# Kernel optimization log

Hardware: AMD Instinct MI355X
Metric: run time of the kernel (lower is better)

## Reference

```python
import jax, jax.numpy as jnp
import numpy as np

B, T, D = 32, 256, 1024      # batch, seq_len, input_size
H = D // 2                   # LSTM hidden size = 512
K = 128                      # num_tags


def setup_inputs() -> dict:
    key = jax.random.key(0)
    ks = jax.random.split(key, 16)
    s_in = 1.0 / np.sqrt(D + K)
    s_h = 1.0 / np.sqrt(H)
    return {
        "hiddens": jax.random.normal(ks[0], (B, T, D), jnp.float32),
        "h_t": jax.random.normal(ks[1], (2, B, H), jnp.float32),
        "c_t": jax.random.normal(ks[2], (2, B, H), jnp.float32),
        "mask": jnp.ones((B, T), jnp.float32),
        # output layer: Linear(H, K)
        "W_out": jax.random.normal(ks[3], (K, H), jnp.float32) * s_h,
        "b_out": jnp.zeros((K,), jnp.float32),
        # LSTM layer 0: input dim = K + D
        "W_ih0": jax.random.normal(ks[4], (4 * H, K + D), jnp.float32) * s_in,
        "W_hh0": jax.random.normal(ks[5], (4 * H, H), jnp.float32) * s_h,
        "b_ih0": jnp.zeros((4 * H,), jnp.float32),
        "b_hh0": jnp.zeros((4 * H,), jnp.float32),
        # LSTM layer 1: input dim = H
        "W_ih1": jax.random.normal(ks[6], (4 * H, H), jnp.float32) * s_h,
        "W_hh1": jax.random.normal(ks[7], (4 * H, H), jnp.float32) * s_h,
        "b_ih1": jnp.zeros((4 * H,), jnp.float32),
        "b_hh1": jnp.zeros((4 * H,), jnp.float32),
    }


def _lstm_cell(x, h, c, W_ih, W_hh, b_ih, b_hh):
    g = x @ W_ih.T + h @ W_hh.T + b_ih + b_hh
    i, f, gg, o = jnp.split(g, 4, axis=-1)
    i = jax.nn.sigmoid(i); f = jax.nn.sigmoid(f)
    gg = jnp.tanh(gg); o = jax.nn.sigmoid(o)
    c = f * c + i * gg
    h = o * jnp.tanh(c)
    return h, c


def reference(hiddens, h_t, c_t, mask, W_out, b_out,
              W_ih0, W_hh0, b_ih0, b_hh0, W_ih1, W_hh1, b_ih1, b_hh1):
    # initial previous-tag distribution from first frame's first half
    last_tag = hiddens[:, 0, :H] @ W_out.T + b_out          # [B,K]
    sm = jax.nn.softmax(last_tag, axis=-1)

    def step(carry, x_t):
        h1, c1, h2, c2, sm = carry
        inp = jnp.concatenate([x_t, sm], axis=-1)           # [B, D+K]
        h1, c1 = _lstm_cell(inp, h1, c1, W_ih0, W_hh0, b_ih0, b_hh0)
        h2, c2 = _lstm_cell(h1, h2, c2, W_ih1, W_hh1, b_ih1, b_hh1)
        logit = h2 @ W_out.T + b_out                        # [B,K]
        sm = jax.nn.softmax(logit, axis=-1)
        return (h1, c1, h2, c2, sm), logit

    carry0 = (h_t[0], c_t[0], h_t[1], c_t[1], sm)
    _, logits_t = jax.lax.scan(step, carry0, jnp.swapaxes(hiddens, 0, 1))  # [T,B,K]
    logits = jnp.swapaxes(logits_t, 0, 1)                   # [B,T,K]
    logits = logits + (1.0 - mask)[:, :, None] * jnp.float32(-1e32)
    prob = jax.nn.softmax(logits, axis=-1)
    return prob
```

## Files before the change

kernel.cpp:

```cpp
#include <hip/hip_runtime.h>
#include <cstdint>
#include <cstddef>


#define Bz   32
#define Tz   256
#define Dz   1024
#define Hz   512
#define NK   128
#define IN0  1152
#define NBLK 256
#define BH   16384

typedef float vf4 __attribute__((ext_vector_type(4)));

__device__ __forceinline__ void ldsc4(vf4& d, const float* p) {
  asm volatile("global_load_dwordx4 %0, %1, off sc0 sc1" : "=v"(d) : "v"(p));
}
__device__ __forceinline__ void ldg1(float& d, const float* p) {
  asm volatile("global_load_dword %0, %1, off" : "=v"(d) : "v"(p));
}
__device__ __forceinline__ void stsc1(float* p, float v) {
  asm volatile("global_store_dword %0, %1, off sc0 sc1" :: "v"(p), "v"(v) : "memory");
}
__device__ __forceinline__ void stsc1u(unsigned int* p, unsigned int v) {
  asm volatile("global_store_dword %0, %1, off sc0 sc1" :: "v"(p), "v"(v) : "memory");
}
#define FENCE8(c, a0,a1,a2,a3,a4,a5,a6,a7) \
  asm volatile("s_waitcnt vmcnt(" #c ")" : "+v"(a0),"+v"(a1),"+v"(a2),"+v"(a3), \
               "+v"(a4),"+v"(a5),"+v"(a6),"+v"(a7) :: "memory")

#define FMA4(acc, W_, A_) \
  acc = fmaf((W_).x,(A_).x, fmaf((W_).y,(A_).y, fmaf((W_).z,(A_).z, fmaf((W_).w,(A_).w,(acc)))))

__device__ __forceinline__ float sigf(float x) { return 1.0f / (1.0f + expf(-x)); }

__device__ __forceinline__ void gbar(unsigned int* slots, unsigned int* bcast,
                                     int gidx, bool master, unsigned int g) {
  asm volatile("s_waitcnt vmcnt(0)" ::: "memory");
  __syncthreads();
  if (threadIdx.x == 0)
    __hip_atomic_store(slots + gidx * 16, g,
                       __ATOMIC_RELAXED, __HIP_MEMORY_SCOPE_SYSTEM);
  if (master) {
    if (threadIdx.x < 128) {
      unsigned int* wsl = slots + threadIdx.x * 16;
      while (__hip_atomic_load(wsl, __ATOMIC_RELAXED, __HIP_MEMORY_SCOPE_SYSTEM) < g)
        __builtin_amdgcn_s_sleep(1);
    }
    __syncthreads();
    if (threadIdx.x == 0) {
      asm volatile("s_waitcnt vmcnt(0)" ::: "memory");
      __hip_atomic_store(bcast, g, __ATOMIC_RELAXED, __HIP_MEMORY_SCOPE_SYSTEM);
    }
  } else if (threadIdx.x == 0) {
    while (__hip_atomic_load(bcast, __ATOMIC_RELAXED, __HIP_MEMORY_SCOPE_SYSTEM) < g)
      __builtin_amdgcn_s_sleep(1);
  }
  __syncthreads();
}

__device__ __forceinline__ void garrive(unsigned int* slots, int gidx,
                                        unsigned int g) {
  asm volatile("s_waitcnt vmcnt(0)" ::: "memory");
  __syncthreads();
  if (threadIdx.x == 0)
    __hip_atomic_store(slots + gidx * 16, g,
                       __ATOMIC_RELAXED, __HIP_MEMORY_SCOPE_SYSTEM);
}

#define FMAROW(r, AV, BASE, KOFF) \
  { vf4 wv = *(const vf4*)&BASE[r][KOFF]; FMA4(A##r, wv, AV); }
#define R16A(OP, AV, BASE, KOFF) \
  OP(0,AV,BASE,KOFF) OP(1,AV,BASE,KOFF) OP(2,AV,BASE,KOFF) OP(3,AV,BASE,KOFF) \
  OP(4,AV,BASE,KOFF) OP(5,AV,BASE,KOFF) OP(6,AV,BASE,KOFF) OP(7,AV,BASE,KOFF) \
  OP(8,AV,BASE,KOFF) OP(9,AV,BASE,KOFF) OP(10,AV,BASE,KOFF) OP(11,AV,BASE,KOFF) \
  OP(12,AV,BASE,KOFF) OP(13,AV,BASE,KOFF) OP(14,AV,BASE,KOFF) OP(15,AV,BASE,KOFF)

#define RED16 { \
  { const bool hi = (ks & 1) != 0; \
    float s0=hi?A0:A8, s1=hi?A1:A9, s2=hi?A2:A10, s3=hi?A3:A11; \
    float s4=hi?A4:A12, s5=hi?A5:A13, s6=hi?A6:A14, s7=hi?A7:A15; \
    float k0=hi?A8:A0, k1=hi?A9:A1, k2=hi?A10:A2, k3=hi?A11:A3; \
    float k4=hi?A12:A4, k5=hi?A13:A5, k6=hi?A14:A6, k7=hi?A15:A7; \
    A0=k0+__shfl_xor(s0,1,64); A1=k1+__shfl_xor(s1,1,64); \
    A2=k2+__shfl_xor(s2,1,64); A3=k3+__shfl_xor(s3,1,64); \
    A4=k4+__shfl_xor(s4,1,64); A5=k5+__shfl_xor(s5,1,64); \
    A6=k6+__shfl_xor(s6,1,64); A7=k7+__shfl_xor(s7,1,64); } \
  { const bool hi = (ks & 2) != 0; \
    float s0=hi?A0:A4, s1=hi?A1:A5, s2=hi?A2:A6, s3=hi?A3:A7; \
    float k0=hi?A4:A0, k1=hi?A5:A1, k2=hi?A6:A2, k3=hi?A7:A3; \
    A0=k0+__shfl_xor(s0,2,64); A1=k1+__shfl_xor(s1,2,64); \
    A2=k2+__shfl_xor(s2,2,64); A3=k3+__shfl_xor(s3,2,64); } \
  { const bool hi = (ks & 4) != 0; \
    float s0=hi?A0:A2, s1=hi?A1:A3; float k0=hi?A2:A0, k1=hi?A3:A1; \
    A0=k0+__shfl_xor(s0,4,64); A1=k1+__shfl_xor(s1,4,64); } \
  { const bool hi = (ks & 8) != 0; \
    float s0=hi?A0:A1; float k0=hi?A1:A0; \
    A0=k0+__shfl_xor(s0,8,64); } }

#define ZERO16 A0=0.f;A1=0.f;A2=0.f;A3=0.f;A4=0.f;A5=0.f;A6=0.f;A7=0.f; \
               A8=0.f;A9=0.f;A10=0.f;A11=0.f;A12=0.f;A13=0.f;A14=0.f;A15=0.f;

#define GATES(CREG, HDST) \
  __syncthreads(); \
  if (tid < 64) { \
    float gi = gbuf[cu][cbl],      gf = gbuf[4 + cu][cbl]; \
    float gg = gbuf[8 + cu][cbl],  go = gbuf[12 + cu][cbl]; \
    CREG = sigf(gf) * CREG + sigf(gi) * tanhf(gg); \
    stsc1(HDST + (size_t)(pg * 16 + cbl) * Hz + jg * 4 + cu, \
          sigf(go) * tanhf(CREG)); \
  }

__device__ void c_head_crit(const float* src, int bb,
                            const float* __restrict__ W_out,
                            const float* __restrict__ b_out,
                            float* __restrict__ smg, float* __restrict__ lggb,
                            float (*cpart)[2], float* wred,
                            unsigned int* smflag, unsigned int fval) {
  const int tid = threadIdx.x;
  const int n = tid & 127, kh = tid >> 7;
  float p = 0.0f;
  const float* w  = W_out + (size_t)n * Hz + kh * 256;
  const float* s2 = src + kh * 256;
  #pragma unroll 8
  for (int k = 0; k < 256; k += 4) {
    vf4 sv = *(const vf4*)(s2 + k);
    vf4 wv = *(const vf4*)(w + k);
    p += sv.x * wv.x + sv.y * wv.y + sv.z * wv.z + sv.w * wv.w;
  }
  cpart[n][kh] = p;
  __syncthreads();
  float logit = 0.0f;
  if (tid < 128) {
    logit = cpart[n][0] + cpart[n][1] + b_out[n];
    stsc1(lggb + n, logit);
  }
  float e = (tid < 128) ? expf(logit) : 0.0f;
  float s = e;
  #pragma unroll
  for (int off = 32; off >= 1; off >>= 1) s += __shfl_xor(s, off);
  if ((tid & 63) == 0 && tid < 128) wred[2 + (tid >> 6)] = s;
  __syncthreads();
  float S = wred[2] + wred[3];
  if (tid < 128) stsc1(smg + bb * NK + n, e / S);
  asm volatile("s_waitcnt vmcnt(0)" ::: "memory");
  __syncthreads();
  if (fval && tid == 0) stsc1u(smflag, fval);
}

__device__ void c_head_out(int t, int bb, const float* __restrict__ mask,
                           float* __restrict__ out,
                           const float* __restrict__ lggb, float* wred) {
  const int tid = threadIdx.x;
  const int n = tid & 127;
  float lg = 0.0f;
  if (tid < 128)
    lg = __hip_atomic_load(lggb + n, __ATOMIC_RELAXED, __HIP_MEMORY_SCOPE_SYSTEM);
  float mk = (tid < 128) ? mask[bb * Tz + t] : 1.0f;
  float lm = (tid < 128) ? (lg + (1.0f - mk) * (-1e32f)) : -3.0e38f;
  float m2 = lm;
  #pragma unroll
  for (int off = 32; off >= 1; off >>= 1) m2 = fmaxf(m2, __shfl_xor(m2, off));
  if ((tid & 63) == 0 && tid < 128) wred[4 + (tid >> 6)] = m2;
  __syncthreads();
  float M2 = fmaxf(wred[4], wred[5]);
  float e2 = (tid < 128) ? expf(lm - M2) : 0.0f;
  float s2r = e2;
  #pragma unroll
  for (int off = 32; off >= 1; off >>= 1) s2r += __shfl_xor(s2r, off);
  if ((tid & 63) == 0 && tid < 128) wred[6 + (tid >> 6)] = s2r;
  __syncthreads();
  float S2 = wred[6] + wred[7];
  if (tid < 128) out[((size_t)bb * Tz + t) * NK + n] = e2 / S2;
}

__global__ void __launch_bounds__(256)
xpre_kernel(const float* __restrict__ hiddens, const float* __restrict__ W_ih0,
            const float* __restrict__ b_ih0, const float* __restrict__ b_hh0,
            float* __restrict__ Xpre, int t0, int colTiles, int cstride) {
  __shared__ float Ws[16][64];
  __shared__ float Hs[16][64];
  const int tid = threadIdx.x;
  const int bx = blockIdx.x % colTiles;
  const int by = blockIdx.x / colTiles;
  const int n0 = by * 64, c0 = bx * 64;
  const int tx = tid & 15, ty = tid >> 4;
  const int ldn = tid >> 2;
  const int ldk = (tid & 3) * 4;

  const int bb = ldn & 31;
  const int tt = t0 + (c0 >> 5) + (ldn >> 5);
  const float* hsrc = hiddens + ((size_t)bb * Tz + tt) * Dz + ldk;
  const float* wsrc = W_ih0 + (size_t)(n0 + ldn) * IN0 + ldk;

  float acc[4][4] = {};
  vf4 wv = *(const vf4*)(wsrc);
  vf4 hv = *(const vf4*)(hsrc);
  for (int k0 = 0; k0 < Dz; k0 += 16) {
    __syncthreads();
    Ws[ldk + 0][ldn] = wv.x; Ws[ldk + 1][ldn] = wv.y;
    Ws[ldk + 2][ldn] = wv.z; Ws[ldk + 3][ldn] = wv.w;
    Hs[ldk + 0][ldn] = hv.x; Hs[ldk + 1][ldn] = hv.y;
    Hs[ldk + 2][ldn] = hv.z; Hs[ldk + 3][ldn] = hv.w;
    __syncthreads();
    if (k0 + 16 < Dz) {
      wv = *(const vf4*)(wsrc + k0 + 16);
      hv = *(const vf4*)(hsrc + k0 + 16);
    }
    #pragma unroll
    for (int k = 0; k < 16; ++k) {
      vf4 a4 = *(const vf4*)&Ws[k][ty * 4];
      vf4 b4 = *(const vf4*)&Hs[k][tx * 4];
      acc[0][0] += a4.x * b4.x; acc[0][1] += a4.x * b4.y; acc[0][2] += a4.x * b4.z; acc[0][3] += a4.x * b4.w;
      acc[1][0] += a4.y * b4.x; acc[1][1] += a4.y * b4.y; acc[1][2] += a4.y * b4.z; acc[1][3] += a4.y * b4.w;
      acc[2][0] += a4.z * b4.x; acc[2][1] += a4.z * b4.y; acc[2][2] += a4.z * b4.z; acc[2][3] += a4.z * b4.w;
      acc[3][0] += a4.w * b4.x; acc[3][1] += a4.w * b4.y; acc[3][2] += a4.w * b4.z; acc[3][3] += a4.w * b4.w;
    }
  }
  #pragma unroll
  for (int i = 0; i < 4; ++i) {
    int n = n0 + ty * 4 + i;
    float bi = b_ih0[n] + b_hh0[n];
    vf4 v; v.x = acc[i][0] + bi; v.y = acc[i][1] + bi;
    v.z = acc[i][2] + bi; v.w = acc[i][3] + bi;
    *(vf4*)(Xpre + (size_t)n * cstride + c0 + tx * 4) = v;
  }
}

__global__ void __launch_bounds__(256)
seq_kernel(const float* __restrict__ hiddens,
           const float* __restrict__ h_t, const float* __restrict__ c_t,
           const float* __restrict__ mask,
           const float* __restrict__ W_out, const float* __restrict__ b_out,
           const float* __restrict__ W_ih0, const float* __restrict__ W_hh0,
           const float* __restrict__ W_ih1, const float* __restrict__ W_hh1,
           const float* __restrict__ b_ih1, const float* __restrict__ b_hh1,
           const float* __restrict__ Xpre, float* __restrict__ out,
           float* __restrict__ h1g, float* __restrict__ h2g,
           float* __restrict__ smg, float* __restrict__ c1g, float* __restrict__ c2g,
           float* __restrict__ lgg,
           unsigned int* bar, int t0, int nsteps, int cstride) {
  __shared__ float wA[16][640];
  __shared__ float wB[16][1024];
  __shared__ float gbuf[16][17];
  __shared__ float biasB[16];
  __shared__ float hsg[512];
  __shared__ float cpart[128][2];
  __shared__ float wred[8];

  const int tid = threadIdx.x;
  const int bid = blockIdx.x;
  const int jg  = bid >> 1;
  const int pg  = bid & 1;
  const int ks  = tid & 15;
  const int bbl = tid >> 4;
  const int bbg = pg * 16 + bbl;
  const int ks4 = ks * 4;
  const int cu  = tid & 3, cbl = tid >> 2;
  const int rr  = ((ks & 1) << 3) | ((ks & 2) << 1) | ((ks & 4) >> 1) | ((ks & 8) >> 3);
  const int rowG = ((rr >> 2) * Hz) + jg * 4 + (rr & 3);
  const int hb = ((bid & 1) << 4) | (bid >> 1);
  const bool isbud = (bid >= 32 && bid < 64);
  const int  bb2   = isbud ? (((bid & 1) << 4) | ((bid >> 1) - 16)) : 0;

  unsigned int* barg = bar + pg * 2048;
  unsigned int* bcst = bar + 4096 + pg * 16;
  unsigned int* smf  = bar + 4608;
  const int  gidx    = bid >> 1;
  const bool gmaster = (gidx == 127);

  #pragma clang loop unroll(disable)
  for (int r = 0; r < 16; ++r) {
    const int row = ((r >> 2) * Hz) + jg * 4 + (r & 3);
    if (tid * 4 < 512)
      *(vf4*)&wA[r][tid * 4] = *(const vf4*)(W_hh0 + (size_t)row * Hz + tid * 4);
    if (tid * 4 < 128)
      *(vf4*)&wA[r][512 + tid * 4] = *(const vf4*)(W_ih0 + (size_t)row * IN0 + 1024 + tid * 4);
    if (tid * 4 < 512) {
      *(vf4*)&wB[r][tid * 4]       = *(const vf4*)(W_ih1 + (size_t)row * Hz + tid * 4);
      *(vf4*)&wB[r][512 + tid * 4] = *(const vf4*)(W_hh1 + (size_t)row * Hz + tid * 4);
    }
  }
  if (tid < 16) {
    const int row = ((tid >> 2) * Hz) + jg * 4 + (tid & 3);
    biasB[tid] = b_ih1[row] + b_hh1[row];
  }

  float c1r = 0.0f, c2r = 0.0f;
  if (tid < 64) {
    const size_t ci = (size_t)(pg * 16 + cbl) * Hz + jg * 4 + cu;
    if (t0 == 0) { c1r = c_t[ci]; c2r = c_t[BH + ci]; }
    else         { c1r = c1g[ci]; c2r = c2g[ci]; }
  }

  if (t0 == 0) {
    if (bid < 32 && tid < 128) {
      vf4 v1 = *(const vf4*)(h_t + (size_t)hb * Hz + tid * 4);
      vf4 v2 = *(const vf4*)(h_t + BH + (size_t)hb * Hz + tid * 4);
      float* d1 = h1g + BH + (size_t)hb * Hz + tid * 4;
      float* d2 = h2g + BH + (size_t)hb * Hz + tid * 4;
      stsc1(d1, v1.x); stsc1(d1 + 1, v1.y); stsc1(d1 + 2, v1.z); stsc1(d1 + 3, v1.w);
      stsc1(d2, v2.x); stsc1(d2 + 1, v2.y); stsc1(d2 + 2, v2.z); stsc1(d2 + 3, v2.w);
    }
    if (bid < 32) {
      if (tid < 128)
        *(vf4*)&hsg[tid * 4] = *(const vf4*)(hiddens + (size_t)hb * Tz * Dz + tid * 4);
      __syncthreads();
      c_head_crit(hsg, hb, W_out, b_out, smg, lgg + hb * NK, cpart, wred,
                  smf + hb * 16, 0u);
    }
  }
  __syncthreads();
  unsigned int g = 1;
  gbar(barg, bcst, gidx, gmaster, g); ++g;

  vf4 ca0,ca1,ca2,ca3,ca4,ca5,ca6,ca7;
  {
    const float* hp = h1g + ((t0 + 1) & 1) * BH + (size_t)bbg * Hz + ks4;
    ldsc4(ca0, hp);        ldsc4(ca1, hp + 64);  ldsc4(ca2, hp + 128);
    ldsc4(ca3, hp + 192);  ldsc4(ca4, hp + 256); ldsc4(ca5, hp + 320);
    ldsc4(ca6, hp + 384);  ldsc4(ca7, hp + 448);
    FENCE8(0, ca0,ca1,ca2,ca3,ca4,ca5,ca6,ca7);
  }

  #pragma clang loop unroll(disable)
  for (int k = 0; k < nsteps; ++k) {
    const int t = t0 + k;
    float*       h1cur  = h1g + (t & 1) * BH;
    const float* h2prev = h2g + ((t + 1) & 1) * BH;
    float*       h2cur  = h2g + (t & 1) * BH;
    float A0,A1,A2,A3,A4,A5,A6,A7,A8,A9,A10,A11,A12,A13,A14,A15;
    vf4 ab0,ab1,ab2,ab3,ab4,ab5,ab6,ab7;

    {
      vf4 as0,as1;
      float xv;
      ldg1(xv, Xpre + (size_t)rowG * cstride + k * 32 + bbg);
      ZERO16
      R16A(FMAROW, ca0, wA, ks4 +   0)
      R16A(FMAROW, ca1, wA, ks4 +  64)
      R16A(FMAROW, ca2, wA, ks4 + 128)
      R16A(FMAROW, ca3, wA, ks4 + 192)
      R16A(FMAROW, ca4, wA, ks4 + 256)
      R16A(FMAROW, ca5, wA, ks4 + 320)
      R16A(FMAROW, ca6, wA, ks4 + 384)
      R16A(FMAROW, ca7, wA, ks4 + 448)
      RED16
      const float partA = A0;
      if (k > 0) {
        const unsigned int tgt = (unsigned int)k;
        if (tid < 16) {
          const unsigned int* fp = smf + (pg * 16 + tid) * 16;
          while (__hip_atomic_load(fp, __ATOMIC_RELAXED,
                                   __HIP_MEMORY_SCOPE_SYSTEM) < tgt)
            __builtin_amdgcn_s_sleep(1);
        }
        __syncthreads();
        if (isbud)
          c_head_out(t - 1, bb2, mask, out, lgg + bb2 * NK, wred);
      }
      const float* sp = smg + (size_t)bbg * NK + ks4;
      ldsc4(as0, sp);        ldsc4(as1, sp + 64);
      ZERO16
      asm volatile("s_waitcnt vmcnt(0)" : "+v"(as0), "+v"(as1), "+v"(xv) :: "memory");
      R16A(FMAROW, as0, wA, ks4 + 512)
      R16A(FMAROW, as1, wA, ks4 + 576)
      RED16
      gbuf[rr][bbl] = partA + A0 + xv;
      GATES(c1r, h1cur)
    }
    {
      const float* p2 = h2prev + (size_t)bbg * Hz + ks4;
      ldsc4(ab0, p2);       ldsc4(ab1, p2 + 64);  ldsc4(ab2, p2 + 128);
      ldsc4(ab3, p2 + 192); ldsc4(ab4, p2 + 256); ldsc4(ab5, p2 + 320);
      ldsc4(ab6, p2 + 384); ldsc4(ab7, p2 + 448);
    }
    const unsigned int gA = g;
    garrive(barg, gidx, gA); ++g;

    {
      ZERO16
      FENCE8(0, ab0,ab1,ab2,ab3,ab4,ab5,ab6,ab7);
      R16A(FMAROW, ab0, wB, ks4 + 512)
      R16A(FMAROW, ab1, wB, ks4 + 576)
      R16A(FMAROW, ab2, wB, ks4 + 640)
      R16A(FMAROW, ab3, wB, ks4 + 704)
      R16A(FMAROW, ab4, wB, ks4 + 768)
      R16A(FMAROW, ab5, wB, ks4 + 832)
      R16A(FMAROW, ab6, wB, ks4 + 896)
      R16A(FMAROW, ab7, wB, ks4 + 960)
      RED16
      const float partB = A0;
      if (gmaster) {
        if (tid < 128) {
          unsigned int* wsl = barg + tid * 16;
          while (__hip_atomic_load(wsl, __ATOMIC_RELAXED,
                                   __HIP_MEMORY_SCOPE_SYSTEM) < gA)
            __builtin_amdgcn_s_sleep(1);
        }
        __syncthreads();
        if (tid == 0)
          __hip_atomic_store(bcst, gA, __ATOMIC_RELAXED, __HIP_MEMORY_SCOPE_SYSTEM);
      } else if (tid == 0) {
        while (__hip_atomic_load(bcst, __ATOMIC_RELAXED,
                                 __HIP_MEMORY_SCOPE_SYSTEM) < gA)
          __builtin_amdgcn_s_sleep(1);
      }
      __syncthreads();
      const float* p1 = h1cur + (size_t)bbg * Hz + ks4;
      ldsc4(ca0, p1);       ldsc4(ca1, p1 + 64);  ldsc4(ca2, p1 + 128);
      ldsc4(ca3, p1 + 192); ldsc4(ca4, p1 + 256); ldsc4(ca5, p1 + 320);
      ldsc4(ca6, p1 + 384); ldsc4(ca7, p1 + 448);
      ZERO16
      FENCE8(0, ca0,ca1,ca2,ca3,ca4,ca5,ca6,ca7);
      R16A(FMAROW, ca0, wB, ks4 +   0)
      R16A(FMAROW, ca1, wB, ks4 +  64)
      R16A(FMAROW, ca2, wB, ks4 + 128)
      R16A(FMAROW, ca3, wB, ks4 + 192)
      R16A(FMAROW, ca4, wB, ks4 + 256)
      R16A(FMAROW, ca5, wB, ks4 + 320)
      R16A(FMAROW, ca6, wB, ks4 + 384)
      R16A(FMAROW, ca7, wB, ks4 + 448)
      RED16
      gbuf[rr][bbl] = A0 + partB + biasB[rr];
      GATES(c2r, h2cur)
    }
    const unsigned int gB = g;
    garrive(barg, gidx, gB); ++g;

    if (bid < 32) {
      if (tid < 128) {
        unsigned int* wsl = barg + tid * 16;
        while (__hip_atomic_load(wsl, __ATOMIC_RELAXED,
                                 __HIP_MEMORY_SCOPE_SYSTEM) < gB)
          __builtin_amdgcn_s_sleep(1);
      }
      __syncthreads();
      if (tid < 128) {
        vf4 v;
        ldsc4(v, h2cur + (size_t)hb * Hz + tid * 4);
        asm volatile("s_waitcnt vmcnt(0)" : "+v"(v) :: "memory");
        *(vf4*)&hsg[tid * 4] = v;
      }
      __syncthreads();
      c_head_crit(hsg, hb, W_out, b_out, smg, lgg + hb * NK, cpart, wred,
                  smf + hb * 16, (unsigned int)(k + 1));
    }
  }

  if (isbud) {
    if (tid == 0) {
      const unsigned int* fp = smf + bb2 * 16;
      while (__hip_atomic_load(fp, __ATOMIC_RELAXED,
                               __HIP_MEMORY_SCOPE_SYSTEM) < (unsigned int)nsteps)
        __builtin_amdgcn_s_sleep(1);
    }
    __syncthreads();
    c_head_out(t0 + nsteps - 1, bb2, mask, out, lgg + bb2 * NK, wred);
  }

  if (tid < 64) {
    const size_t ci = (size_t)(pg * 16 + cbl) * Hz + jg * 4 + cu;
    stsc1(c1g + ci, c1r);
    stsc1(c2g + ci, c2r);
  }
}

extern "C" void kernel_launch(void* const* d_in, const int* in_sizes, int n_in,
                              void* d_out, int out_size, void* d_ws, size_t ws_size,
                              hipStream_t stream) {
  (void)in_sizes; (void)n_in; (void)out_size;
  const float* hiddens = (const float*)d_in[0];
  const float* h_t     = (const float*)d_in[1];
  const float* c_t     = (const float*)d_in[2];
  const float* mask    = (const float*)d_in[3];
  const float* W_out   = (const float*)d_in[4];
  const float* b_out   = (const float*)d_in[5];
  const float* W_ih0   = (const float*)d_in[6];
  const float* W_hh0   = (const float*)d_in[7];
  const float* b_ih0   = (const float*)d_in[8];
  const float* b_hh0   = (const float*)d_in[9];
  const float* W_ih1   = (const float*)d_in[10];
  const float* W_hh1   = (const float*)d_in[11];
  const float* b_ih1   = (const float*)d_in[12];
  const float* b_hh1   = (const float*)d_in[13];
  float* out = (float*)d_out;

  unsigned int* bar = (unsigned int*)d_ws;
  float* base = (float*)((char*)d_ws + 32768);
  float* h1g  = base;
  float* h2g  = h1g + 2 * BH;
  float* smg  = h2g + 2 * BH;
  float* c1g  = smg + Bz * NK;
  float* c2g  = c1g + BH;
  float* lgg  = c2g + BH;
  float* Xpre = lgg + Bz * NK;

  const size_t fullNeed = 32768 + (size_t)(102400 + Bz * NK + 2048 * 8192) * 4;
  const bool full = ws_size >= fullNeed;
  const int NCH    = full ? 1 : 16;
  const int CH     = full ? Tz : 16;
  const int cstr   = full ? (Tz * 32) : (16 * 32);
  const int cTiles = cstr / 64;

  for (int c = 0; c < NCH; ++c) {
    const int t0 = c * CH;
    hipMemsetAsync(bar, 0, 32768, stream);
    hipLaunchKernelGGL(xpre_kernel, dim3(32 * cTiles), dim3(256), 0, stream,
                       hiddens, W_ih0, b_ih0, b_hh0, Xpre, t0, cTiles, cstr);
    int nsteps = CH, cs = cstr, tt0 = t0;
    void* ka[] = { (void*)&hiddens, (void*)&h_t, (void*)&c_t, (void*)&mask,
                   (void*)&W_out, (void*)&b_out, (void*)&W_ih0, (void*)&W_hh0,
                   (void*)&W_ih1, (void*)&W_hh1, (void*)&b_ih1, (void*)&b_hh1,
                   (void*)&Xpre, (void*)&out, (void*)&h1g, (void*)&h2g,
                   (void*)&smg, (void*)&c1g, (void*)&c2g, (void*)&lgg,
                   (void*)&bar, (void*)&tt0, (void*)&nsteps, (void*)&cs };
    hipError_t err = hipLaunchCooperativeKernel((void*)seq_kernel, dim3(NBLK),
                                                dim3(256), ka, 0, stream);
    if (err != hipSuccess) {
      hipLaunchKernelGGL(seq_kernel, dim3(NBLK), dim3(256), 0, stream,
                         hiddens, h_t, c_t, mask, W_out, b_out, W_ih0, W_hh0,
                         W_ih1, W_hh1, b_ih1, b_hh1, Xpre, out,
                         h1g, h2g, smg, c1g, c2g, lgg, bar, tt0, nsteps, cs);
    }
  }
}
```

Before: 5.256 ms.

## Defer softmax normalization into layer-0 gate input via packed flag+sum

The head block now writes unnormalized exp(logit) values and the softmax denominator. The denominator is packed into the 64-bit ready flag next to the step counter. Consumers read the sum along with the flag and scale their partial dot product by 1/S, which takes the division and a block barrier off the critical head path. The head's dot-product reduction also uses a lane shuffle instead of shared memory plus __syncthreads. The risk is that exp(logit) without max subtraction can overflow, and the 64-bit flag store must be atomic.

```diff
diff --git a/kernel.cpp b/kernel.cpp
--- a/kernel.cpp
+++ b/kernel.cpp
@@ -13,6 +13,7 @@
 #define BH   16384
 
 typedef float vf4 __attribute__((ext_vector_type(4)));
+typedef unsigned long long ull;
 
 __device__ __forceinline__ void ldsc4(vf4& d, const float* p) {
   asm volatile("global_load_dwordx4 %0, %1, off sc0 sc1" : "=v"(d) : "v"(p));
@@ -20,11 +21,17 @@
 __device__ __forceinline__ void ldg1(float& d, const float* p) {
   asm volatile("global_load_dword %0, %1, off" : "=v"(d) : "v"(p));
 }
+__device__ __forceinline__ float ldsc1f(const float* p) {
+  float d;
+  asm volatile("global_load_dword %0, %1, off sc0 sc1" : "=v"(d) : "v"(p));
+  asm volatile("s_waitcnt vmcnt(0)" : "+v"(d) :: "memory");
+  return d;
+}
 __device__ __forceinline__ void stsc1(float* p, float v) {
   asm volatile("global_store_dword %0, %1, off sc0 sc1" :: "v"(p), "v"(v) : "memory");
 }
-__device__ __forceinline__ void stsc1u(unsigned int* p, unsigned int v) {
-  asm volatile("global_store_dword %0, %1, off sc0 sc1" :: "v"(p), "v"(v) : "memory");
+__device__ __forceinline__ void stsc2u(ull* p, ull v) {
+  asm volatile("global_store_dwordx2 %0, %1, off sc0 sc1" :: "v"(p), "v"(v) : "memory");
 }
 #define FENCE8(c, a0,a1,a2,a3,a4,a5,a6,a7) \
   asm volatile("s_waitcnt vmcnt(" #c ")" : "+v"(a0),"+v"(a1),"+v"(a2),"+v"(a3), \
@@ -116,10 +123,10 @@
                             const float* __restrict__ W_out,
                             const float* __restrict__ b_out,
                             float* __restrict__ smg, float* __restrict__ lggb,
-                            float (*cpart)[2], float* wred,
-                            unsigned int* smflag, unsigned int fval) {
+                            float* __restrict__ sSb, float* wred,
+                            ull* smflag64, unsigned int fval) {
   const int tid = threadIdx.x;
-  const int n = tid & 127, kh = tid >> 7;
+  const int n = tid >> 1, kh = tid & 1;
   float p = 0.0f;
   const float* w  = W_out + (size_t)n * Hz + kh * 256;
   const float* s2 = src + kh * 256;
@@ -129,24 +136,26 @@
     vf4 wv = *(const vf4*)(w + k);
     p += sv.x * wv.x + sv.y * wv.y + sv.z * wv.z + sv.w * wv.w;
   }
-  cpart[n][kh] = p;
-  __syncthreads();
-  float logit = 0.0f;
-  if (tid < 128) {
-    logit = cpart[n][0] + cpart[n][1] + b_out[n];
+  p += __shfl_xor(p, 1, 64);
+  float logit = p + b_out[n];
+  float e = expf(logit);
+  if (kh == 0) {
     stsc1(lggb + n, logit);
-  }
-  float e = (tid < 128) ? expf(logit) : 0.0f;
+    stsc1(smg + bb * NK + n, e);
+  }
   float s = e;
   #pragma unroll
   for (int off = 32; off >= 1; off >>= 1) s += __shfl_xor(s, off);
-  if ((tid & 63) == 0 && tid < 128) wred[2 + (tid >> 6)] = s;
-  __syncthreads();
-  float S = wred[2] + wred[3];
-  if (tid < 128) stsc1(smg + bb * NK + n, e / S);
+  if ((tid & 63) == 0) wred[tid >> 6] = s;
+  __syncthreads();
+  float S = (wred[0] + wred[1] + wred[2] + wred[3]) * 0.5f;
+  if (tid == 0) stsc1(sSb, S);
   asm volatile("s_waitcnt vmcnt(0)" ::: "memory");
   __syncthreads();
-  if (fval && tid == 0) stsc1u(smflag, fval);
+  if (fval && tid == 0) {
+    ull v = ((ull)fval << 32) | (ull)__float_as_uint(S);
+    stsc2u(smflag64, v);
+  }
 }
 
 __device__ void c_head_out(int t, int bb, const float* __restrict__ mask,
@@ -239,15 +248,15 @@
            const float* __restrict__ Xpre, float* __restrict__ out,
            float* __restrict__ h1g, float* __restrict__ h2g,
            float* __restrict__ smg, float* __restrict__ c1g, float* __restrict__ c2g,
-           float* __restrict__ lgg,
+           float* __restrict__ lgg, float* __restrict__ sSg,
            unsigned int* bar, int t0, int nsteps, int cstride) {
   __shared__ float wA[16][640];
   __shared__ float wB[16][1024];
   __shared__ float gbuf[16][17];
   __shared__ float biasB[16];
   __shared__ float hsg[512];
-  __shared__ float cpart[128][2];
   __shared__ float wred[8];
+  __shared__ float sSl[16];
 
   const int tid = threadIdx.x;
   const int bid = blockIdx.x;
@@ -307,8 +316,8 @@
       if (tid < 128)
         *(vf4*)&hsg[tid * 4] = *(const vf4*)(hiddens + (size_t)hb * Tz * Dz + tid * 4);
       __syncthreads();
-      c_head_crit(hsg, hb, W_out, b_out, smg, lgg + hb * NK, cpart, wred,
-                  smf + hb * 16, 0u);
+      c_head_crit(hsg, hb, W_out, b_out, smg, lgg + hb * NK, sSg + hb, wred,
+                  (ull*)(smf + hb * 16), 0u);
     }
   }
   __syncthreads();
@@ -351,14 +360,21 @@
       if (k > 0) {
         const unsigned int tgt = (unsigned int)k;
         if (tid < 16) {
-          const unsigned int* fp = smf + (pg * 16 + tid) * 16;
-          while (__hip_atomic_load(fp, __ATOMIC_RELAXED,
-                                   __HIP_MEMORY_SCOPE_SYSTEM) < tgt)
+          const ull* fp = (const ull*)(smf + (pg * 16 + tid) * 16);
+          ull v;
+          for (;;) {
+            v = __hip_atomic_load(fp, __ATOMIC_RELAXED, __HIP_MEMORY_SCOPE_SYSTEM);
+            if ((unsigned int)(v >> 32) >= tgt) break;
             __builtin_amdgcn_s_sleep(1);
+          }
+          sSl[tid] = 1.0f / __uint_as_float((unsigned int)v);
         }
         __syncthreads();
         if (isbud)
           c_head_out(t - 1, bb2, mask, out, lgg + bb2 * NK, wred);
+      } else {
+        if (tid < 16) sSl[tid] = 1.0f / ldsc1f(sSg + pg * 16 + tid);
+        __syncthreads();
       }
       const float* sp = smg + (size_t)bbg * NK + ks4;
       ldsc4(as0, sp);        ldsc4(as1, sp + 64);
@@ -367,7 +383,7 @@
       R16A(FMAROW, as0, wA, ks4 + 512)
       R16A(FMAROW, as1, wA, ks4 + 576)
       RED16
-      gbuf[rr][bbl] = partA + A0 + xv;
+      gbuf[rr][bbl] = partA + A0 * sSl[bbl] + xv;
       GATES(c1r, h1cur)
     }
     {
@@ -444,16 +460,16 @@
         *(vf4*)&hsg[tid * 4] = v;
       }
       __syncthreads();
-      c_head_crit(hsg, hb, W_out, b_out, smg, lgg + hb * NK, cpart, wred,
-                  smf + hb * 16, (unsigned int)(k + 1));
+      c_head_crit(hsg, hb, W_out, b_out, smg, lgg + hb * NK, sSg + hb, wred,
+                  (ull*)(smf + hb * 16), (unsigned int)(k + 1));
     }
   }
 
   if (isbud) {
     if (tid == 0) {
-      const unsigned int* fp = smf + bb2 * 16;
-      while (__hip_atomic_load(fp, __ATOMIC_RELAXED,
-                               __HIP_MEMORY_SCOPE_SYSTEM) < (unsigned int)nsteps)
+      const ull* fp = (const ull*)(smf + bb2 * 16);
+      while ((unsigned int)(__hip_atomic_load(fp, __ATOMIC_RELAXED,
+                              __HIP_MEMORY_SCOPE_SYSTEM) >> 32) < (unsigned int)nsteps)
         __builtin_amdgcn_s_sleep(1);
     }
     __syncthreads();
@@ -495,9 +511,10 @@
   float* c1g  = smg + Bz * NK;
   float* c2g  = c1g + BH;
   float* lgg  = c2g + BH;
-  float* Xpre = lgg + Bz * NK;
-
-  const size_t fullNeed = 32768 + (size_t)(102400 + Bz * NK + 2048 * 8192) * 4;
+  float* sSg  = lgg + Bz * NK;
+  float* Xpre = sSg + 64;
+
+  const size_t fullNeed = 32768 + (size_t)(102400 + Bz * NK + 64 + 2048 * 8192) * 4;
   const bool full = ws_size >= fullNeed;
   const int NCH    = full ? 1 : 16;
   const int CH     = full ? Tz : 16;
@@ -515,14 +532,15 @@
                    (void*)&W_ih1, (void*)&W_hh1, (void*)&b_ih1, (void*)&b_hh1,
                    (void*)&Xpre, (void*)&out, (void*)&h1g, (void*)&h2g,
                    (void*)&smg, (void*)&c1g, (void*)&c2g, (void*)&lgg,
-                   (void*)&bar, (void*)&tt0, (void*)&nsteps, (void*)&cs };
+                   (void*)&sSg, (void*)&bar, (void*)&tt0, (void*)&nsteps,
+                   (void*)&cs };
     hipError_t err = hipLaunchCooperativeKernel((void*)seq_kernel, dim3(NBLK),
                                                 dim3(256), ka, 0, stream);
     if (err != hipSuccess) {
       hipLaunchKernelGGL(seq_kernel, dim3(NBLK), dim3(256), 0, stream,
                          hiddens, h_t, c_t, mask, W_out, b_out, W_ih0, W_hh0,
                          W_ih1, W_hh1, b_ih1, b_hh1, Xpre, out,
-                         h1g, h2g, smg, c1g, c2g, lgg, bar, tt0, nsteps, cs);
-    }
-  }
-}
+                         h1g, h2g, smg, c1g, c2g, lgg, sSg, bar, tt0, nsteps, cs);
+    }
+  }
+}
```

Measured after the change: 5.196 ms. About the same (-1.1%).

## Pack softmax numerators with flag and sum into polled slots, drop barrier broadcast

Applied to the files above, without the earlier changes.

The head now writes unnormalized exp values into 8-float slots, each holding a step flag and the softmax sum. Consumers poll those slots directly, so the separate flag poll, block sync and second softmax load are gone, and normalization moves to a multiply by 1/S inside the layer-0 dot product. The head's two-half dot product is reduced with a lane shuffle instead of shared memory. The master/broadcast barrier stage is replaced by every block polling all 128 slots itself, which removes one hop but adds more polling traffic. Correctness depends on each 8-byte flag+sum store landing atomically and on the exp values landing before the flag, and on the per-thread spin loops staying consistent across the block.

```diff
diff --git a/kernel.cpp b/kernel.cpp
--- a/kernel.cpp
+++ b/kernel.cpp
@@ -13,6 +13,7 @@
 #define BH   16384
 
 typedef float vf4 __attribute__((ext_vector_type(4)));
+typedef unsigned long long ull;
 
 __device__ __forceinline__ void ldsc4(vf4& d, const float* p) {
   asm volatile("global_load_dwordx4 %0, %1, off sc0 sc1" : "=v"(d) : "v"(p));
@@ -23,8 +24,8 @@
 __device__ __forceinline__ void stsc1(float* p, float v) {
   asm volatile("global_store_dword %0, %1, off sc0 sc1" :: "v"(p), "v"(v) : "memory");
 }
-__device__ __forceinline__ void stsc1u(unsigned int* p, unsigned int v) {
-  asm volatile("global_store_dword %0, %1, off sc0 sc1" :: "v"(p), "v"(v) : "memory");
+__device__ __forceinline__ void stsc2u(ull* p, ull v) {
+  asm volatile("global_store_dwordx2 %0, %1, off sc0 sc1" :: "v"(p), "v"(v) : "memory");
 }
 #define FENCE8(c, a0,a1,a2,a3,a4,a5,a6,a7) \
   asm volatile("s_waitcnt vmcnt(" #c ")" : "+v"(a0),"+v"(a1),"+v"(a2),"+v"(a3), \
@@ -115,11 +116,11 @@
 __device__ void c_head_crit(const float* src, int bb,
                             const float* __restrict__ W_out,
                             const float* __restrict__ b_out,
-                            float* __restrict__ smg, float* __restrict__ lggb,
-                            float (*cpart)[2], float* wred,
-                            unsigned int* smflag, unsigned int fval) {
+                            float* __restrict__ esl, float* __restrict__ lggb,
+                            float* wred, unsigned int fval) {
   const int tid = threadIdx.x;
-  const int n = tid & 127, kh = tid >> 7;
+  const int n = tid >> 1, kh = tid & 1;
+  float* eslb = esl + (size_t)bb * 256;
   float p = 0.0f;
   const float* w  = W_out + (size_t)n * Hz + kh * 256;
   const float* s2 = src + kh * 256;
@@ -129,24 +130,25 @@
     vf4 wv = *(const vf4*)(w + k);
     p += sv.x * wv.x + sv.y * wv.y + sv.z * wv.z + sv.w * wv.w;
   }
-  cpart[n][kh] = p;
-  __syncthreads();
-  float logit = 0.0f;
-  if (tid < 128) {
-    logit = cpart[n][0] + cpart[n][1] + b_out[n];
+  p += __shfl_xor(p, 1, 64);
+  float logit = p + b_out[n];
+  float e = expf(logit);
+  if (kh == 0) {
     stsc1(lggb + n, logit);
-  }
-  float e = (tid < 128) ? expf(logit) : 0.0f;
+    stsc1(eslb + (n >> 2) * 8 + 2 + (n & 3), e);
+  }
   float s = e;
   #pragma unroll
   for (int off = 32; off >= 1; off >>= 1) s += __shfl_xor(s, off);
-  if ((tid & 63) == 0 && tid < 128) wred[2 + (tid >> 6)] = s;
-  __syncthreads();
-  float S = wred[2] + wred[3];
-  if (tid < 128) stsc1(smg + bb * NK + n, e / S);
+  if ((tid & 63) == 0) wred[tid >> 6] = s;
+  __syncthreads();
+  float S = (wred[0] + wred[1] + wred[2] + wred[3]) * 0.5f;
   asm volatile("s_waitcnt vmcnt(0)" ::: "memory");
   __syncthreads();
-  if (fval && tid == 0) stsc1u(smflag, fval);
+  if (tid < 32) {
+    ull v = ((ull)__float_as_uint(S) << 32) | (ull)fval;
+    stsc2u((ull*)(eslb + tid * 8), v);
+  }
 }
 
 __device__ void c_head_out(int t, int bb, const float* __restrict__ mask,
@@ -238,7 +240,7 @@
            const float* __restrict__ b_ih1, const float* __restrict__ b_hh1,
            const float* __restrict__ Xpre, float* __restrict__ out,
            float* __restrict__ h1g, float* __restrict__ h2g,
-           float* __restrict__ smg, float* __restrict__ c1g, float* __restrict__ c2g,
+           float* __restrict__ esl, float* __restrict__ c1g, float* __restrict__ c2g,
            float* __restrict__ lgg,
            unsigned int* bar, int t0, int nsteps, int cstride) {
   __shared__ float wA[16][640];
@@ -246,7 +248,6 @@
   __shared__ float gbuf[16][17];
   __shared__ float biasB[16];
   __shared__ float hsg[512];
-  __shared__ float cpart[128][2];
   __shared__ float wred[8];
 
   const int tid = threadIdx.x;
@@ -266,9 +267,11 @@
 
   unsigned int* barg = bar + pg * 2048;
   unsigned int* bcst = bar + 4096 + pg * 16;
-  unsigned int* smf  = bar + 4608;
   const int  gidx    = bid >> 1;
   const bool gmaster = (gidx == 127);
+
+  const float* slotA = esl + (size_t)bbg * 256 + (size_t)ks * 8;
+  const float* slotB = esl + (size_t)bbg * 256 + (size_t)(16 + ks) * 8;
 
   #pragma clang loop unroll(disable)
   for (int r = 0; r < 16; ++r) {
@@ -307,8 +310,7 @@
       if (tid < 128)
         *(vf4*)&hsg[tid * 4] = *(const vf4*)(hiddens + (size_t)hb * Tz * Dz + tid * 4);
       __syncthreads();
-      c_head_crit(hsg, hb, W_out, b_out, smg, lgg + hb * NK, cpart, wred,
-                  smf + hb * 16, 0u);
+      c_head_crit(hsg, hb, W_out, b_out, esl, lgg + hb * NK, wred, 0u);
     }
   }
   __syncthreads();
@@ -334,7 +336,6 @@
     vf4 ab0,ab1,ab2,ab3,ab4,ab5,ab6,ab7;
 
     {
-      vf4 as0,as1;
       float xv;
       ldg1(xv, Xpre + (size_t)rowG * cstride + k * 32 + bbg);
       ZERO16
@@ -348,26 +349,36 @@
       R16A(FMAROW, ca7, wA, ks4 + 448)
       RED16
       const float partA = A0;
+      vf4 pa0, pa1, pb0, pb1;
       if (k > 0) {
         const unsigned int tgt = (unsigned int)k;
-        if (tid < 16) {
-          const unsigned int* fp = smf + (pg * 16 + tid) * 16;
-          while (__hip_atomic_load(fp, __ATOMIC_RELAXED,
-                                   __HIP_MEMORY_SCOPE_SYSTEM) < tgt)
-            __builtin_amdgcn_s_sleep(1);
+        for (;;) {
+          ldsc4(pa0, slotA); ldsc4(pa1, slotA + 4);
+          ldsc4(pb0, slotB); ldsc4(pb1, slotB + 4);
+          asm volatile("s_waitcnt vmcnt(0)"
+                       : "+v"(pa0), "+v"(pa1), "+v"(pb0), "+v"(pb1) :: "memory");
+          if (__float_as_uint(pa0.x) >= tgt && __float_as_uint(pb0.x) >= tgt)
+            break;
+          __builtin_amdgcn_s_sleep(2);
         }
-        __syncthreads();
         if (isbud)
           c_head_out(t - 1, bb2, mask, out, lgg + bb2 * NK, wred);
+      } else {
+        ldsc4(pa0, slotA); ldsc4(pa1, slotA + 4);
+        ldsc4(pb0, slotB); ldsc4(pb1, slotB + 4);
+        asm volatile("s_waitcnt vmcnt(0)"
+                     : "+v"(pa0), "+v"(pa1), "+v"(pb0), "+v"(pb1) :: "memory");
       }
-      const float* sp = smg + (size_t)bbg * NK + ks4;
-      ldsc4(as0, sp);        ldsc4(as1, sp + 64);
+      asm volatile("s_waitcnt vmcnt(0)" : "+v"(xv) :: "memory");
+      const float invS = 1.0f / pa0.y;
+      vf4 as0, as1;
+      as0.x = pa0.z; as0.y = pa0.w; as0.z = pa1.x; as0.w = pa1.y;
+      as1.x = pb0.z; as1.y = pb0.w; as1.z = pb1.x; as1.w = pb1.y;
       ZERO16
-      asm volatile("s_waitcnt vmcnt(0)" : "+v"(as0), "+v"(as1), "+v"(xv) :: "memory");
       R16A(FMAROW, as0, wA, ks4 + 512)
       R16A(FMAROW, as1, wA, ks4 + 576)
       RED16
-      gbuf[rr][bbl] = partA + A0 + xv;
+      gbuf[rr][bbl] = partA + A0 * invS + xv;
       GATES(c1r, h1cur)
     }
     {
@@ -392,18 +403,9 @@
       R16A(FMAROW, ab7, wB, ks4 + 960)
       RED16
       const float partB = A0;
-      if (gmaster) {
-        if (tid < 128) {
-          unsigned int* wsl = barg + tid * 16;
-          while (__hip_atomic_load(wsl, __ATOMIC_RELAXED,
-                                   __HIP_MEMORY_SCOPE_SYSTEM) < gA)
-            __builtin_amdgcn_s_sleep(1);
-        }
-        __syncthreads();
-        if (tid == 0)
-          __hip_atomic_store(bcst, gA, __ATOMIC_RELAXED, __HIP_MEMORY_SCOPE_SYSTEM);
-      } else if (tid == 0) {
-        while (__hip_atomic_load(bcst, __ATOMIC_RELAXED,
+      if (tid < 128) {
+        unsigned int* wsl = barg + tid * 16;
+        while (__hip_atomic_load(wsl, __ATOMIC_RELAXED,
                                  __HIP_MEMORY_SCOPE_SYSTEM) < gA)
           __builtin_amdgcn_s_sleep(1);
       }
@@ -444,14 +446,14 @@
         *(vf4*)&hsg[tid * 4] = v;
       }
       __syncthreads();
-      c_head_crit(hsg, hb, W_out, b_out, smg, lgg + hb * NK, cpart, wred,
-                  smf + hb * 16, (unsigned int)(k + 1));
+      c_head_crit(hsg, hb, W_out, b_out, esl, lgg + hb * NK, wred,
+                  (unsigned int)(k + 1));
     }
   }
 
   if (isbud) {
     if (tid == 0) {
-      const unsigned int* fp = smf + bb2 * 16;
+      const unsigned int* fp = (const unsigned int*)(esl + (size_t)bb2 * 256);
       while (__hip_atomic_load(fp, __ATOMIC_RELAXED,
                                __HIP_MEMORY_SCOPE_SYSTEM) < (unsigned int)nsteps)
         __builtin_amdgcn_s_sleep(1);
@@ -491,13 +493,14 @@
   float* base = (float*)((char*)d_ws + 32768);
   float* h1g  = base;
   float* h2g  = h1g + 2 * BH;
-  float* smg  = h2g + 2 * BH;
-  float* c1g  = smg + Bz * NK;
+  float* esl  = h2g + 2 * BH;
+  float* c1g  = esl + Bz * 256;
   float* c2g  = c1g + BH;
   float* lgg  = c2g + BH;
   float* Xpre = lgg + Bz * NK;
 
-  const size_t fullNeed = 32768 + (size_t)(102400 + Bz * NK + 2048 * 8192) * 4;
+  const size_t fullNeed = 32768 +
+      (size_t)(4 * BH + Bz * 256 + 2 * BH + Bz * NK + 2048 * 8192) * 4;
   const bool full = ws_size >= fullNeed;
   const int NCH    = full ? 1 : 16;
   const int CH     = full ? Tz : 16;
@@ -514,7 +517,7 @@
                    (void*)&W_out, (void*)&b_out, (void*)&W_ih0, (void*)&W_hh0,
                    (void*)&W_ih1, (void*)&W_hh1, (void*)&b_ih1, (void*)&b_hh1,
                    (void*)&Xpre, (void*)&out, (void*)&h1g, (void*)&h2g,
-                   (void*)&smg, (void*)&c1g, (void*)&c2g, (void*)&lgg,
+                   (void*)&esl, (void*)&c1g, (void*)&c2g, (void*)&lgg,
                    (void*)&bar, (void*)&tt0, (void*)&nsteps, (void*)&cs };
     hipError_t err = hipLaunchCooperativeKernel((void*)seq_kernel, dim3(NBLK),
                                                 dim3(256), ka, 0, stream);
@@ -522,7 +525,7 @@
       hipLaunchKernelGGL(seq_kernel, dim3(NBLK), dim3(256), 0, stream,
                          hiddens, h_t, c_t, mask, W_out, b_out, W_ih0, W_hh0,
                          W_ih1, W_hh1, b_ih1, b_hh1, Xpre, out,
-                         h1g, h2g, smg, c1g, c2g, lgg, bar, tt0, nsteps, cs);
-    }
-  }
-}
+                         h1g, h2g, esl, c1g, c2g, lgg, bar, tt0, nsteps, cs);
+    }
+  }
+}
```

New measurement: 5.395 ms. 2.6% more time.
